# Kernel optimization log

Measured on AMD Instinct MI355X. Metric: run time of the kernel, lower is better.

Reference implementation:

```python
import jax, jax.numpy as jnp
import numpy as np

S, B, H, V, L = 128, 32, 512, 10000, 2

def setup_inputs() -> dict:
    key = jax.random.key(0)
    ks = jax.random.split(key, 8)
    u = float(np.sqrt(1.0 / H))
    return {
        "tokens": jax.random.randint(ks[0], (S, B), 0, V, dtype=jnp.int64),
        "h0": jnp.zeros((L, B, H), dtype=jnp.float32),
        "emb": jax.random.normal(ks[1], (V, H), dtype=jnp.float32) * 0.1,
        "Wx": jax.random.uniform(ks[2], (L, 3, H, H), minval=-u, maxval=u, dtype=jnp.float32),
        "bx": jax.random.uniform(ks[3], (L, 3, H), minval=-u, maxval=u, dtype=jnp.float32),
        "U": jax.random.uniform(ks[4], (L, 3, H, H), minval=-u, maxval=u, dtype=jnp.float32),
        "Wy": jax.random.uniform(ks[5], (V, H), minval=-u, maxval=u, dtype=jnp.float32),
        "by": jax.random.uniform(ks[6], (V,), minval=-u, maxval=u, dtype=jnp.float32),
    }

def _gru_cell(x, h, Wx, bx, U):
    # x,h: [B,H]; Wx,U: [3,H,H]; bx: [3,H]
    ax = jnp.einsum('bi,gio->bgo', x, Wx) + bx  # [B,3,H]
    r = jax.nn.sigmoid(ax[:, 0] + h @ U[0])
    z = jax.nn.sigmoid(ax[:, 1] + h @ U[1])
    h_hat = jnp.tanh(ax[:, 2] + (r * h) @ U[2])
    return (1.0 - z) * h + z * h_hat

def reference(tokens, h0, emb, Wx, bx, U, Wy, by):
    embs = emb[tokens]  # [S,B,H]

    def step(h_stack, x_t):
        new_h = []
        inp = x_t
        for l in range(L):
            h_l = _gru_cell(inp, h_stack[l], Wx[l], bx[l], U[l])
            new_h.append(h_l)
            inp = h_l
        return jnp.stack(new_h), inp  # carry, top-layer output

    h_final, tops = jax.lax.scan(step, h0, embs)  # tops: [S,B,H]
    logits = jnp.einsum('sbh,vh->sbv', tops, Wy) + by  # [S,B,V]
    return logits, h_final
```

## Files before the change

### kernel.cpp

```cpp
#include <hip/hip_runtime.h>
#include <cmath>

#define S_LEN 128
#define BATCH 32
#define HID   512
#define VOCAB 10000
#define MROWS (S_LEN * BATCH)
#define HH    (HID * HID)

#define NBLK  64
#define NTHR  512

typedef float f32x4 __attribute__((ext_vector_type(4)));

template<bool GATHER_A, bool B_KN, bool C_T>
__global__ __launch_bounds__(256) void gemm_kernel(
    const float* __restrict__ A, const int* __restrict__ tok,
    const float* __restrict__ Bmat, const float* __restrict__ bias,
    float* __restrict__ C, int M, int N, int K)
{
    __shared__ float As[32][68];
    __shared__ float Bs[32][68];
    __shared__ int   toks[64];

    const int tid = threadIdx.x;
    const int m0  = blockIdx.y * 64;
    const int n0  = blockIdx.x * 64;

    if (GATHER_A && tid < 64) toks[tid] = tok[m0 + tid];
    __syncthreads();

    const int tx = tid & 15;
    const int ty = tid >> 4;
    const int lr = tid >> 3;
    const int lc = (tid & 7) * 4;

    float acc[4][4] = {};

    for (int k0 = 0; k0 < K; k0 += 32) {
        #pragma unroll
        for (int rep = 0; rep < 2; rep++) {
            int r = lr + rep * 32;
            const float* arow;
            if (GATHER_A) arow = A + (size_t)toks[r] * K;
            else          arow = A + (size_t)(m0 + r) * K;
            float4 v = *(const float4*)(arow + k0 + lc);
            As[lc + 0][r] = v.x; As[lc + 1][r] = v.y;
            As[lc + 2][r] = v.z; As[lc + 3][r] = v.w;
        }
        if (B_KN) {
            int g    = n0 >> 9;
            int col0 = n0 & 511;
            const float* bbase = Bmat + (size_t)g * K * 512 + col0;
            int bc = (tid & 15) * 4;
            int bk = tid >> 4;
            #pragma unroll
            for (int rep = 0; rep < 2; rep++) {
                int kk = bk + rep * 16;
                float4 v = *(const float4*)(bbase + (size_t)(k0 + kk) * 512 + bc);
                *(float4*)&Bs[kk][bc] = v;
            }
        } else {
            #pragma unroll
            for (int rep = 0; rep < 2; rep++) {
                int r = lr + rep * 32;
                int n = n0 + r;
                float4 v = make_float4(0.f, 0.f, 0.f, 0.f);
                if (n < N) v = *(const float4*)(Bmat + (size_t)n * K + k0 + lc);
                Bs[lc + 0][r] = v.x; Bs[lc + 1][r] = v.y;
                Bs[lc + 2][r] = v.z; Bs[lc + 3][r] = v.w;
            }
        }
        __syncthreads();
        #pragma unroll
        for (int k = 0; k < 32; k++) {
            float4 a4 = *(const float4*)&As[k][ty * 4];
            float4 b4 = *(const float4*)&Bs[k][tx * 4];
            float av[4] = {a4.x, a4.y, a4.z, a4.w};
            float bv[4] = {b4.x, b4.y, b4.z, b4.w};
            #pragma unroll
            for (int i = 0; i < 4; i++)
                #pragma unroll
                for (int j = 0; j < 4; j++)
                    acc[i][j] = fmaf(av[i], bv[j], acc[i][j]);
        }
        __syncthreads();
    }
    if (C_T) {
        #pragma unroll
        for (int j = 0; j < 4; j++) {
            int n = n0 + tx * 4 + j;
            float bn = bias[n];
            float4 v = make_float4(acc[0][j] + bn, acc[1][j] + bn,
                                   acc[2][j] + bn, acc[3][j] + bn);
            *(float4*)&C[(size_t)n * M + m0 + ty * 4] = v;
        }
    } else {
        #pragma unroll
        for (int i = 0; i < 4; i++) {
            int m = m0 + ty * 4 + i;
            #pragma unroll
            for (int j = 0; j < 4; j++) {
                int n = n0 + tx * 4 + j;
                if (n < N) C[(size_t)m * N + n] = acc[i][j] + bias[n];
            }
        }
    }
}

__global__ __launch_bounds__(256) void gemm128_kernel(
    const float* __restrict__ A, const float* __restrict__ B,
    const float* __restrict__ bias, float* __restrict__ C,
    int M, int N, int K)
{
    __shared__ float As[16][132];
    __shared__ float Bs[16][132];

    const int tid = threadIdx.x;
    const int m0  = blockIdx.y * 128;
    const int n0  = blockIdx.x * 128;
    const int tx  = tid & 15;
    const int ty  = tid >> 4;
    const int lr  = tid >> 2;
    const int lc  = (tid & 3) * 4;

    float acc[8][8] = {};

    for (int k0 = 0; k0 < K; k0 += 16) {
        #pragma unroll
        for (int rep = 0; rep < 2; rep++) {
            int r = lr + rep * 64;
            float4 va = *(const float4*)(A + (size_t)(m0 + r) * K + k0 + lc);
            As[lc + 0][r] = va.x; As[lc + 1][r] = va.y;
            As[lc + 2][r] = va.z; As[lc + 3][r] = va.w;
            int n = n0 + r;
            float4 vb = make_float4(0.f, 0.f, 0.f, 0.f);
            if (n < N) vb = *(const float4*)(B + (size_t)n * K + k0 + lc);
            Bs[lc + 0][r] = vb.x; Bs[lc + 1][r] = vb.y;
            Bs[lc + 2][r] = vb.z; Bs[lc + 3][r] = vb.w;
        }
        __syncthreads();
        #pragma unroll
        for (int k = 0; k < 16; k++) {
            f32x4 a0 = *(const f32x4*)&As[k][ty * 8];
            f32x4 a1 = *(const f32x4*)&As[k][ty * 8 + 4];
            f32x4 b0 = *(const f32x4*)&Bs[k][tx * 8];
            f32x4 b1 = *(const f32x4*)&Bs[k][tx * 8 + 4];
            float av[8] = {a0.x,a0.y,a0.z,a0.w,a1.x,a1.y,a1.z,a1.w};
            float bv[8] = {b0.x,b0.y,b0.z,b0.w,b1.x,b1.y,b1.z,b1.w};
            #pragma unroll
            for (int i = 0; i < 8; i++)
                #pragma unroll
                for (int j = 0; j < 8; j++)
                    acc[i][j] = fmaf(av[i], bv[j], acc[i][j]);
        }
        __syncthreads();
    }
    const bool full = (n0 + 128 <= N);
    #pragma unroll
    for (int i = 0; i < 8; i++) {
        int m = m0 + ty * 8 + i;
        if (full) {
            int n = n0 + tx * 8;
            float4 v0 = make_float4(acc[i][0]+bias[n+0], acc[i][1]+bias[n+1],
                                    acc[i][2]+bias[n+2], acc[i][3]+bias[n+3]);
            float4 v1 = make_float4(acc[i][4]+bias[n+4], acc[i][5]+bias[n+5],
                                    acc[i][6]+bias[n+6], acc[i][7]+bias[n+7]);
            *(float4*)&C[(size_t)m * N + n]     = v0;
            *(float4*)&C[(size_t)m * N + n + 4] = v1;
        } else {
            #pragma unroll
            for (int j = 0; j < 8; j++) {
                int n = n0 + tx * 8 + j;
                if (n < N) C[(size_t)m * N + n] = acc[i][j] + bias[n];
            }
        }
    }
}

__device__ __forceinline__ f32x4 ldg_coh_x4(const float* p) {
    f32x4 r;
    asm volatile("global_load_dwordx4 %0, %1, off sc1"
                 : "=v"(r) : "v"(p) : "memory");
    return r;
}
__device__ __forceinline__ void stg_coh(float* p, float v) {
    asm volatile("global_store_dword %0, %1, off sc1"
                 :: "v"(p), "v"(v) : "memory");
}

__device__ __forceinline__ void bar_arrive(unsigned* flags, int bid, unsigned target)
{
    asm volatile("s_waitcnt vmcnt(0)" ::: "memory");
    __syncthreads();
    if (threadIdx.x == 0)
        __hip_atomic_store(&flags[bid], target, __ATOMIC_RELEASE, __HIP_MEMORY_SCOPE_AGENT);
}
__device__ __forceinline__ void bar_wait(unsigned* flags, unsigned target)
{
    if (threadIdx.x < NBLK) {
        while (__hip_atomic_load(&flags[threadIdx.x], __ATOMIC_RELAXED,
                                 __HIP_MEMORY_SCOPE_AGENT) < target)
            __builtin_amdgcn_s_sleep(1);
    }
    __syncthreads();
}

__global__ __launch_bounds__(NTHR) void scan_coop_kernel(
    const float* __restrict__ axT, const float* __restrict__ Ul,
    const float* __restrict__ h0g, float* __restrict__ hseq,
    float* __restrict__ hfin, float* __restrict__ vT,
    float* __restrict__ hxT, unsigned* __restrict__ flags)
{
    __shared__ float Wr[512 * 8];
    __shared__ float Wz[512 * 8];
    __shared__ float Wh[512 * 8];
    __shared__ float xbuf[512 * 32];
    __shared__ float part[32 * 256];
    __shared__ float partR[8 * 256];
    __shared__ float zbuf[8 * 33];
    __shared__ float hsave[8 * 33];
    __shared__ float hnb[8 * 33];

    const int tid = threadIdx.x;
    const int bid = blockIdx.x;
    const int ch0 = bid << 3;

    const int bt  = tid & 7;
    const int ct1 = (tid >> 3) & 1;
    const int ks  = tid >> 4;
    const int wsel = ((ct1 ^ ks) & 1) << 2;
    const int rc  = tid >> 5;
    const int rb  = tid & 31;

    for (int idx = tid; idx < 512 * 8; idx += NTHR) {
        int c = idx & 7, k = idx >> 3;
        int p = (k << 3) + ((((c >> 2) ^ (k >> 4)) & 1) << 2) + (c & 3);
        Wr[p] = Ul[                (size_t)k * HID + ch0 + c];
        Wz[p] = Ul[(size_t)1 * HH + (size_t)k * HID + ch0 + c];
        Wh[p] = Ul[(size_t)2 * HH + (size_t)k * HID + ch0 + c];
    }

    if (tid < 256)
        stg_coh(hxT + (ch0 + rc) * 32 + rb, h0g[rb * HID + ch0 + rc]);
    unsigned bc = 1;
    bar_arrive(flags, bid, bc);

    float axr = 0.f, axz = 0.f, axh = 0.f;
    if (tid < 256) {
        axr = axT[(size_t)(       ch0 + rc) * MROWS + rb];
        axz = axT[(size_t)( 512 + ch0 + rc) * MROWS + rb];
        axh = axT[(size_t)(1024 + ch0 + rc) * MROWS + rb];
    }
    bar_wait(flags, bc); bc++;

    for (int t = 0; t < S_LEN; t++) {
        {
            f32x4 ld[8];
            #pragma unroll
            for (int i = 0; i < 8; i++)
                ld[i] = ldg_coh_x4(hxT + (size_t)(tid + i * NTHR) * 4);
            asm volatile("s_waitcnt vmcnt(0)" ::: "memory");
            #pragma unroll
            for (int i = 0; i < 8; i++)
                *(f32x4*)&xbuf[(tid + i * NTHR) * 4] = ld[i];
        }
        __syncthreads();

        {
            f32x4 a0 = {0.f,0.f,0.f,0.f}, a1 = a0, a2 = a0, a3 = a0;
            const int kb = ks << 4;
            #pragma unroll
            for (int kk = 0; kk < 16; kk++) {
                int k = kb + kk;
                f32x4 wv = *(const f32x4*)&Wr[(k << 3) + wsel];
                f32x4 xv = *(const f32x4*)&xbuf[(k << 5) + (bt << 2)];
                a0 += wv.x * xv; a1 += wv.y * xv;
                a2 += wv.z * xv; a3 += wv.w * xv;
            }
            const int c0 = ct1 << 2;
            *(f32x4*)&part[(ks << 8) + ((c0    ) << 5) + (bt << 2)] = a0;
            *(f32x4*)&part[(ks << 8) + ((c0 + 1) << 5) + (bt << 2)] = a1;
            *(f32x4*)&part[(ks << 8) + ((c0 + 2) << 5) + (bt << 2)] = a2;
            *(f32x4*)&part[(ks << 8) + ((c0 + 3) << 5) + (bt << 2)] = a3;
        }
        __syncthreads();
        {
            const int out4 = tid & 63, qh = tid >> 6;
            f32x4 s = {0.f,0.f,0.f,0.f};
            #pragma unroll
            for (int j = 0; j < 4; j++)
                s += *(const f32x4*)&part[(((qh << 2) + j) << 8) + (out4 << 2)];
            *(f32x4*)&partR[(qh << 8) + (out4 << 2)] = s;
        }
        __syncthreads();
        if (tid < 256) {
            float s = 0.f;
            #pragma unroll
            for (int qh = 0; qh < 8; qh++) s += partR[(qh << 8) + (rc << 5) + rb];
            float sig = 1.f / (1.f + __expf(-(axr + s)));
            float hk  = xbuf[((ch0 + rc) << 5) + rb];
            stg_coh(vT + (ch0 + rc) * 32 + rb, sig * hk);
        }
        bar_arrive(flags, bid, bc);

        {
            f32x4 a0 = {0.f,0.f,0.f,0.f}, a1 = a0, a2 = a0, a3 = a0;
            const int kb = ks << 4;
            #pragma unroll
            for (int kk = 0; kk < 16; kk++) {
                int k = kb + kk;
                f32x4 wv = *(const f32x4*)&Wz[(k << 3) + wsel];
                f32x4 xv = *(const f32x4*)&xbuf[(k << 5) + (bt << 2)];
                a0 += wv.x * xv; a1 += wv.y * xv;
                a2 += wv.z * xv; a3 += wv.w * xv;
            }
            const int c0 = ct1 << 2;
            *(f32x4*)&part[(ks << 8) + ((c0    ) << 5) + (bt << 2)] = a0;
            *(f32x4*)&part[(ks << 8) + ((c0 + 1) << 5) + (bt << 2)] = a1;
            *(f32x4*)&part[(ks << 8) + ((c0 + 2) << 5) + (bt << 2)] = a2;
            *(f32x4*)&part[(ks << 8) + ((c0 + 3) << 5) + (bt << 2)] = a3;
        }
        __syncthreads();
        {
            const int out4 = tid & 63, qh = tid >> 6;
            f32x4 s = {0.f,0.f,0.f,0.f};
            #pragma unroll
            for (int j = 0; j < 4; j++)
                s += *(const f32x4*)&part[(((qh << 2) + j) << 8) + (out4 << 2)];
            *(f32x4*)&partR[(qh << 8) + (out4 << 2)] = s;
        }
        __syncthreads();
        if (tid < 256) {
            float s = 0.f;
            #pragma unroll
            for (int qh = 0; qh < 8; qh++) s += partR[(qh << 8) + (rc << 5) + rb];
            zbuf[rc * 33 + rb]  = 1.f / (1.f + __expf(-(axz + s)));
            hsave[rc * 33 + rb] = xbuf[((ch0 + rc) << 5) + rb];
        }
        bar_wait(flags, bc); bc++;

        {
            f32x4 ld[8];
            #pragma unroll
            for (int i = 0; i < 8; i++)
                ld[i] = ldg_coh_x4(vT + (size_t)(tid + i * NTHR) * 4);
            asm volatile("s_waitcnt vmcnt(0)" ::: "memory");
            #pragma unroll
            for (int i = 0; i < 8; i++)
                *(f32x4*)&xbuf[(tid + i * NTHR) * 4] = ld[i];
        }
        __syncthreads();

        {
            f32x4 a0 = {0.f,0.f,0.f,0.f}, a1 = a0, a2 = a0, a3 = a0;
            const int kb = ks << 4;
            #pragma unroll
            for (int kk = 0; kk < 16; kk++) {
                int k = kb + kk;
                f32x4 wv = *(const f32x4*)&Wh[(k << 3) + wsel];
                f32x4 xv = *(const f32x4*)&xbuf[(k << 5) + (bt << 2)];
                a0 += wv.x * xv; a1 += wv.y * xv;
                a2 += wv.z * xv; a3 += wv.w * xv;
            }
            const int c0 = ct1 << 2;
            *(f32x4*)&part[(ks << 8) + ((c0    ) << 5) + (bt << 2)] = a0;
            *(f32x4*)&part[(ks << 8) + ((c0 + 1) << 5) + (bt << 2)] = a1;
            *(f32x4*)&part[(ks << 8) + ((c0 + 2) << 5) + (bt << 2)] = a2;
            *(f32x4*)&part[(ks << 8) + ((c0 + 3) << 5) + (bt << 2)] = a3;
        }
        __syncthreads();
        {
            const int out4 = tid & 63, qh = tid >> 6;
            f32x4 s = {0.f,0.f,0.f,0.f};
            #pragma unroll
            for (int j = 0; j < 4; j++)
                s += *(const f32x4*)&part[(((qh << 2) + j) << 8) + (out4 << 2)];
            *(f32x4*)&partR[(qh << 8) + (out4 << 2)] = s;
        }
        __syncthreads();
        if (tid < 256) {
            float s = 0.f;
            #pragma unroll
            for (int qh = 0; qh < 8; qh++) s += partR[(qh << 8) + (rc << 5) + rb];
            float pre = axh + s;
            float e2  = __expf(2.f * pre);
            float hh  = 1.f - 2.f / (e2 + 1.f);
            float z   = zbuf[rc * 33 + rb];
            float h   = hsave[rc * 33 + rb];
            float hn  = (1.f - z) * h + z * hh;
            stg_coh(hxT + (ch0 + rc) * 32 + rb, hn);
            hnb[rc * 33 + rb] = hn;
            if (t == S_LEN - 1) hfin[rb * HID + ch0 + rc] = hn;
        }
        bar_arrive(flags, bid, bc);

        if (tid < 256) {
            const int c2 = tid & 7, b2 = tid >> 3;
            hseq[(size_t)((t << 5) + b2) * HID + ch0 + c2] = hnb[c2 * 33 + b2];
            if (t + 1 < S_LEN) {
                const size_t o = (size_t)((t + 1) << 5) + rb;
                axr = axT[(size_t)(       ch0 + rc) * MROWS + o];
                axz = axT[(size_t)( 512 + ch0 + rc) * MROWS + o];
                axh = axT[(size_t)(1024 + ch0 + rc) * MROWS + o];
            }
        }
        bar_wait(flags, bc); bc++;
    }
}

extern "C" void kernel_launch(void* const* d_in, const int* in_sizes, int n_in,
                              void* d_out, int out_size, void* d_ws, size_t ws_size,
                              hipStream_t stream)
{
    const int*   tokens = (const int*)  d_in[0];
    const float* h0     = (const float*)d_in[1];
    const float* emb    = (const float*)d_in[2];
    const float* Wx     = (const float*)d_in[3];
    const float* bx     = (const float*)d_in[4];
    const float* U      = (const float*)d_in[5];
    const float* Wy     = (const float*)d_in[6];
    const float* by     = (const float*)d_in[7];
    float*       out    = (float*)d_out;

    float* ws    = (float*)d_ws;
    float* axT   = ws;
    float* hseq  = axT + (size_t)1536 * MROWS;

    const size_t logits_sz = (size_t)MROWS * VOCAB;
    float* hfin0 = out + logits_sz;
    float* hfin1 = out + logits_sz + BATCH * HID;

    float*    vT    = out;
    float*    hxT   = out + 16384;
    unsigned* flags = (unsigned*)(out + 32768);
    hipMemsetAsync(flags, 0, 2 * NBLK * sizeof(unsigned), stream);

    gemm_kernel<true, true, true><<<dim3(1536 / 64, MROWS / 64), 256, 0, stream>>>(
        emb, tokens, Wx, bx, axT, MROWS, 1536, HID);

    scan_coop_kernel<<<NBLK, NTHR, 0, stream>>>(
        axT, U, h0, hseq, hfin0, vT, hxT, flags);

    gemm_kernel<false, true, true><<<dim3(1536 / 64, MROWS / 64), 256, 0, stream>>>(
        hseq, nullptr, Wx + 3 * HH, bx + 1536, axT, MROWS, 1536, HID);

    scan_coop_kernel<<<NBLK, NTHR, 0, stream>>>(
        axT, U + 3 * HH, h0 + BATCH * HID, hseq, hfin1, vT, hxT, flags + NBLK);

    gemm128_kernel<<<dim3((VOCAB + 127) / 128, MROWS / 128), 256, 0, stream>>>(
        hseq, Wy, by, out, MROWS, VOCAB, HID);
}
```

Before: 3.453 ms.

## Spread recurrent scan over 128 blocks and unify GEMMs on swizzled 128x128 tiles

The cooperative scan kernel now runs on 128 blocks that each own 4 hidden channels instead of 64 blocks owning 8. Each block does half the recurrent dot-product work per step, and the reductions are reorganized into 64 k-slices. The input-projection GEMMs move from 64x64 to 128x128 tiles via one templated kernel, with an XOR swizzle on the B shared-memory tile to reduce bank conflicts. The wider scan increases the number of blocks polling the flag barrier each step, and the larger GEMM tiles launch fewer blocks.

```diff
diff --git a/kernel.cpp b/kernel.cpp
--- a/kernel.cpp
+++ b/kernel.cpp
@@ -8,144 +8,84 @@
 #define MROWS (S_LEN * BATCH)
 #define HH    (HID * HID)
 
-#define NBLK  64
+#define NBLK  128
 #define NTHR  512
 
 typedef float f32x4 __attribute__((ext_vector_type(4)));
 
 template<bool GATHER_A, bool B_KN, bool C_T>
-__global__ __launch_bounds__(256) void gemm_kernel(
+__global__ __launch_bounds__(256) void gemm128_kernel(
     const float* __restrict__ A, const int* __restrict__ tok,
     const float* __restrict__ Bmat, const float* __restrict__ bias,
     float* __restrict__ C, int M, int N, int K)
 {
-    __shared__ float As[32][68];
-    __shared__ float Bs[32][68];
-    __shared__ int   toks[64];
+    __shared__ float As[16][132];
+    __shared__ float Bs[16][132];
+    __shared__ int   toks[128];
 
     const int tid = threadIdx.x;
-    const int m0  = blockIdx.y * 64;
-    const int n0  = blockIdx.x * 64;
-
-    if (GATHER_A && tid < 64) toks[tid] = tok[m0 + tid];
-    __syncthreads();
+    const int m0  = blockIdx.y * 128;
+    const int n0  = blockIdx.x * 128;
+
+    if (GATHER_A) {
+        if (tid < 128) toks[tid] = tok[m0 + tid];
+        __syncthreads();
+    }
 
     const int tx = tid & 15;
     const int ty = tid >> 4;
-    const int lr = tid >> 3;
-    const int lc = (tid & 7) * 4;
-
-    float acc[4][4] = {};
-
-    for (int k0 = 0; k0 < K; k0 += 32) {
+    const int lr = tid >> 2;
+    const int lc = (tid & 3) * 4;
+
+    const int qb   = tx << 1;
+    const int bbit = (qb >> 3) & 1;
+    const int bq0  = ((qb    ) ^ bbit) << 2;
+    const int bq1  = ((qb + 1) ^ bbit) << 2;
+
+    float acc[8][8] = {};
+
+    for (int k0 = 0; k0 < K; k0 += 16) {
         #pragma unroll
         for (int rep = 0; rep < 2; rep++) {
-            int r = lr + rep * 32;
-            const float* arow;
-            if (GATHER_A) arow = A + (size_t)toks[r] * K;
-            else          arow = A + (size_t)(m0 + r) * K;
-            float4 v = *(const float4*)(arow + k0 + lc);
-            As[lc + 0][r] = v.x; As[lc + 1][r] = v.y;
-            As[lc + 2][r] = v.z; As[lc + 3][r] = v.w;
+            int r = lr + rep * 64;
+            const float* arow = GATHER_A ? A + (size_t)toks[r] * K
+                                         : A + (size_t)(m0 + r) * K;
+            float4 va = *(const float4*)(arow + k0 + lc);
+            As[lc + 0][r] = va.x; As[lc + 1][r] = va.y;
+            As[lc + 2][r] = va.z; As[lc + 3][r] = va.w;
         }
         if (B_KN) {
-            int g    = n0 >> 9;
-            int col0 = n0 & 511;
-            const float* bbase = Bmat + (size_t)g * K * 512 + col0;
-            int bc = (tid & 15) * 4;
-            int bk = tid >> 4;
+            const int g = n0 >> 9, col0 = n0 & 511;
+            const float* bb = Bmat + (size_t)g * K * 512 + col0;
+            const int q  = tid & 31;
+            const int pq = (q ^ ((q >> 3) & 1)) << 2;
+            const int bkh = tid >> 5;
             #pragma unroll
             for (int rep = 0; rep < 2; rep++) {
-                int kk = bk + rep * 16;
-                float4 v = *(const float4*)(bbase + (size_t)(k0 + kk) * 512 + bc);
-                *(float4*)&Bs[kk][bc] = v;
+                int kk = bkh + rep * 8;
+                float4 vb = *(const float4*)(bb + (size_t)(k0 + kk) * 512 + q * 4);
+                *(float4*)&Bs[kk][pq] = vb;
             }
         } else {
             #pragma unroll
             for (int rep = 0; rep < 2; rep++) {
-                int r = lr + rep * 32;
+                int r = lr + rep * 64;
                 int n = n0 + r;
-                float4 v = make_float4(0.f, 0.f, 0.f, 0.f);
-                if (n < N) v = *(const float4*)(Bmat + (size_t)n * K + k0 + lc);
-                Bs[lc + 0][r] = v.x; Bs[lc + 1][r] = v.y;
-                Bs[lc + 2][r] = v.z; Bs[lc + 3][r] = v.w;
+                float4 vb = make_float4(0.f, 0.f, 0.f, 0.f);
+                if (n < N) vb = *(const float4*)(Bmat + (size_t)n * K + k0 + lc);
+                int q  = r >> 2;
+                int pc = ((q ^ ((q >> 3) & 1)) << 2) + (r & 3);
+                Bs[lc + 0][pc] = vb.x; Bs[lc + 1][pc] = vb.y;
+                Bs[lc + 2][pc] = vb.z; Bs[lc + 3][pc] = vb.w;
             }
-        }
-        __syncthreads();
-        #pragma unroll
-        for (int k = 0; k < 32; k++) {
-            float4 a4 = *(const float4*)&As[k][ty * 4];
-            float4 b4 = *(const float4*)&Bs[k][tx * 4];
-            float av[4] = {a4.x, a4.y, a4.z, a4.w};
-            float bv[4] = {b4.x, b4.y, b4.z, b4.w};
-            #pragma unroll
-            for (int i = 0; i < 4; i++)
-                #pragma unroll
-                for (int j = 0; j < 4; j++)
-                    acc[i][j] = fmaf(av[i], bv[j], acc[i][j]);
-        }
-        __syncthreads();
-    }
-    if (C_T) {
-        #pragma unroll
-        for (int j = 0; j < 4; j++) {
-            int n = n0 + tx * 4 + j;
-            float bn = bias[n];
-            float4 v = make_float4(acc[0][j] + bn, acc[1][j] + bn,
-                                   acc[2][j] + bn, acc[3][j] + bn);
-            *(float4*)&C[(size_t)n * M + m0 + ty * 4] = v;
-        }
-    } else {
-        #pragma unroll
-        for (int i = 0; i < 4; i++) {
-            int m = m0 + ty * 4 + i;
-            #pragma unroll
-            for (int j = 0; j < 4; j++) {
-                int n = n0 + tx * 4 + j;
-                if (n < N) C[(size_t)m * N + n] = acc[i][j] + bias[n];
-            }
-        }
-    }
-}
-
-__global__ __launch_bounds__(256) void gemm128_kernel(
-    const float* __restrict__ A, const float* __restrict__ B,
-    const float* __restrict__ bias, float* __restrict__ C,
-    int M, int N, int K)
-{
-    __shared__ float As[16][132];
-    __shared__ float Bs[16][132];
-
-    const int tid = threadIdx.x;
-    const int m0  = blockIdx.y * 128;
-    const int n0  = blockIdx.x * 128;
-    const int tx  = tid & 15;
-    const int ty  = tid >> 4;
-    const int lr  = tid >> 2;
-    const int lc  = (tid & 3) * 4;
-
-    float acc[8][8] = {};
-
-    for (int k0 = 0; k0 < K; k0 += 16) {
-        #pragma unroll
-        for (int rep = 0; rep < 2; rep++) {
-            int r = lr + rep * 64;
-            float4 va = *(const float4*)(A + (size_t)(m0 + r) * K + k0 + lc);
-            As[lc + 0][r] = va.x; As[lc + 1][r] = va.y;
-            As[lc + 2][r] = va.z; As[lc + 3][r] = va.w;
-            int n = n0 + r;
-            float4 vb = make_float4(0.f, 0.f, 0.f, 0.f);
-            if (n < N) vb = *(const float4*)(B + (size_t)n * K + k0 + lc);
-            Bs[lc + 0][r] = vb.x; Bs[lc + 1][r] = vb.y;
-            Bs[lc + 2][r] = vb.z; Bs[lc + 3][r] = vb.w;
         }
         __syncthreads();
         #pragma unroll
         for (int k = 0; k < 16; k++) {
             f32x4 a0 = *(const f32x4*)&As[k][ty * 8];
             f32x4 a1 = *(const f32x4*)&As[k][ty * 8 + 4];
-            f32x4 b0 = *(const f32x4*)&Bs[k][tx * 8];
-            f32x4 b1 = *(const f32x4*)&Bs[k][tx * 8 + 4];
+            f32x4 b0 = *(const f32x4*)&Bs[k][bq0];
+            f32x4 b1 = *(const f32x4*)&Bs[k][bq1];
             float av[8] = {a0.x,a0.y,a0.z,a0.w,a1.x,a1.y,a1.z,a1.w};
             float bv[8] = {b0.x,b0.y,b0.z,b0.w,b1.x,b1.y,b1.z,b1.w};
             #pragma unroll
@@ -156,23 +96,38 @@
         }
         __syncthreads();
     }
-    const bool full = (n0 + 128 <= N);
-    #pragma unroll
-    for (int i = 0; i < 8; i++) {
-        int m = m0 + ty * 8 + i;
-        if (full) {
-            int n = n0 + tx * 8;
-            float4 v0 = make_float4(acc[i][0]+bias[n+0], acc[i][1]+bias[n+1],
-                                    acc[i][2]+bias[n+2], acc[i][3]+bias[n+3]);
-            float4 v1 = make_float4(acc[i][4]+bias[n+4], acc[i][5]+bias[n+5],
-                                    acc[i][6]+bias[n+6], acc[i][7]+bias[n+7]);
-            *(float4*)&C[(size_t)m * N + n]     = v0;
-            *(float4*)&C[(size_t)m * N + n + 4] = v1;
-        } else {
-            #pragma unroll
-            for (int j = 0; j < 8; j++) {
-                int n = n0 + tx * 8 + j;
-                if (n < N) C[(size_t)m * N + n] = acc[i][j] + bias[n];
+    if (C_T) {
+        #pragma unroll
+        for (int j = 0; j < 8; j++) {
+            int n = n0 + tx * 8 + j;
+            float bn_ = bias[n];
+            float4 v0 = make_float4(acc[0][j]+bn_, acc[1][j]+bn_,
+                                    acc[2][j]+bn_, acc[3][j]+bn_);
+            float4 v1 = make_float4(acc[4][j]+bn_, acc[5][j]+bn_,
+                                    acc[6][j]+bn_, acc[7][j]+bn_);
+            float* cp = C + (size_t)n * M + m0 + ty * 8;
+            *(float4*)cp       = v0;
+            *(float4*)(cp + 4) = v1;
+        }
+    } else {
+        const bool full = (n0 + 128 <= N);
+        #pragma unroll
+        for (int i = 0; i < 8; i++) {
+            int m = m0 + ty * 8 + i;
+            if (full) {
+                int n = n0 + tx * 8;
+                float4 v0 = make_float4(acc[i][0]+bias[n+0], acc[i][1]+bias[n+1],
+                                        acc[i][2]+bias[n+2], acc[i][3]+bias[n+3]);
+                float4 v1 = make_float4(acc[i][4]+bias[n+4], acc[i][5]+bias[n+5],
+                                        acc[i][6]+bias[n+6], acc[i][7]+bias[n+7]);
+                *(float4*)&C[(size_t)m * N + n]     = v0;
+                *(float4*)&C[(size_t)m * N + n + 4] = v1;
+            } else {
+                #pragma unroll
+                for (int j = 0; j < 8; j++) {
+                    int n = n0 + tx * 8 + j;
+                    if (n < N) C[(size_t)m * N + n] = acc[i][j] + bias[n];
+                }
             }
         }
     }
@@ -212,177 +167,123 @@
     float* __restrict__ hfin, float* __restrict__ vT,
     float* __restrict__ hxT, unsigned* __restrict__ flags)
 {
-    __shared__ float Wr[512 * 8];
-    __shared__ float Wz[512 * 8];
-    __shared__ float Wh[512 * 8];
-    __shared__ float xbuf[512 * 32];
-    __shared__ float part[32 * 256];
-    __shared__ float partR[8 * 256];
-    __shared__ float zbuf[8 * 33];
-    __shared__ float hsave[8 * 33];
-    __shared__ float hnb[8 * 33];
+    __shared__ float Wr[HID * 4];
+    __shared__ float Wz[HID * 4];
+    __shared__ float Wh[HID * 4];
+    __shared__ float xbuf[HID * 32];
+    __shared__ float part[64 * 128];
+    __shared__ float partR[16 * 128];
+    __shared__ float zbuf[4 * 33];
+    __shared__ float hsave[4 * 33];
+    __shared__ float hnb[4 * 33];
 
     const int tid = threadIdx.x;
     const int bid = blockIdx.x;
-    const int ch0 = bid << 3;
-
-    const int bt  = tid & 7;
-    const int ct1 = (tid >> 3) & 1;
-    const int ks  = tid >> 4;
-    const int wsel = ((ct1 ^ ks) & 1) << 2;
-    const int rc  = tid >> 5;
-    const int rb  = tid & 31;
-
-    for (int idx = tid; idx < 512 * 8; idx += NTHR) {
-        int c = idx & 7, k = idx >> 3;
-        int p = (k << 3) + ((((c >> 2) ^ (k >> 4)) & 1) << 2) + (c & 3);
-        Wr[p] = Ul[                (size_t)k * HID + ch0 + c];
-        Wz[p] = Ul[(size_t)1 * HH + (size_t)k * HID + ch0 + c];
-        Wh[p] = Ul[(size_t)2 * HH + (size_t)k * HID + ch0 + c];
-    }
-
-    if (tid < 256)
+    const int ch0 = bid << 2;
+
+    const int bt   = tid & 7;
+    const int ks   = tid >> 3;
+    const int out4 = tid & 31;
+    const int qh   = tid >> 5;
+    const int rc   = tid >> 5;
+    const int rb   = tid & 31;
+
+    for (int idx = tid; idx < HID * 4; idx += NTHR) {
+        int c = idx & 3, k = idx >> 2;
+        Wr[idx] = Ul[                 (size_t)k * HID + ch0 + c];
+        Wz[idx] = Ul[(size_t)1 * HH + (size_t)k * HID + ch0 + c];
+        Wh[idx] = Ul[(size_t)2 * HH + (size_t)k * HID + ch0 + c];
+    }
+
+    if (tid < 128)
         stg_coh(hxT + (ch0 + rc) * 32 + rb, h0g[rb * HID + ch0 + rc]);
     unsigned bc = 1;
     bar_arrive(flags, bid, bc);
 
     float axr = 0.f, axz = 0.f, axh = 0.f;
-    if (tid < 256) {
+    if (tid < 128) {
         axr = axT[(size_t)(       ch0 + rc) * MROWS + rb];
         axz = axT[(size_t)( 512 + ch0 + rc) * MROWS + rb];
         axh = axT[(size_t)(1024 + ch0 + rc) * MROWS + rb];
     }
     bar_wait(flags, bc); bc++;
 
+#define DOT(W) {                                                          \
+    f32x4 a0 = {0.f,0.f,0.f,0.f}, a1 = a0, a2 = a0, a3 = a0;              \
+    const float* wb = (W) + (ks << 5);                                    \
+    const float* xb = xbuf + (ks << 8) + (bt << 2);                       \
+    _Pragma("unroll")                                                     \
+    for (int kk = 0; kk < 8; kk++) {                                      \
+        f32x4 wv = *(const f32x4*)(wb + (kk << 2));                       \
+        f32x4 xv = *(const f32x4*)(xb + (kk << 5));                       \
+        a0 += wv.x * xv; a1 += wv.y * xv;                                 \
+        a2 += wv.z * xv; a3 += wv.w * xv;                                 \
+    }                                                                     \
+    float* pp = part + (ks << 7) + (bt << 2);                             \
+    *(f32x4*)(pp     ) = a0;                                              \
+    *(f32x4*)(pp + 32) = a1;                                              \
+    *(f32x4*)(pp + 64) = a2;                                              \
+    *(f32x4*)(pp + 96) = a3; }
+
+#define RED1 {                                                            \
+    f32x4 s = {0.f,0.f,0.f,0.f};                                          \
+    _Pragma("unroll")                                                     \
+    for (int jj = 0; jj < 4; jj++)                                        \
+        s += *(const f32x4*)&part[(((qh << 2) + jj) << 7) + (out4 << 2)]; \
+    *(f32x4*)&partR[(qh << 7) + (out4 << 2)] = s; }
+
+#define RED2(dst) {                                                       \
+    float s_ = 0.f;                                                       \
+    _Pragma("unroll")                                                     \
+    for (int q_ = 0; q_ < 16; q_++) s_ += partR[(q_ << 7) + tid];         \
+    dst = s_; }
+
+#define STAGE(src) {                                                      \
+    f32x4 ld[8];                                                          \
+    _Pragma("unroll")                                                     \
+    for (int i = 0; i < 8; i++)                                           \
+        ld[i] = ldg_coh_x4((src) + (size_t)(tid + i * NTHR) * 4);         \
+    asm volatile("s_waitcnt vmcnt(0)" ::: "memory");                      \
+    _Pragma("unroll")                                                     \
+    for (int i = 0; i < 8; i++)                                           \
+        *(f32x4*)&xbuf[(tid + i * NTHR) * 4] = ld[i]; }
+
     for (int t = 0; t < S_LEN; t++) {
-        {
-            f32x4 ld[8];
-            #pragma unroll
-            for (int i = 0; i < 8; i++)
-                ld[i] = ldg_coh_x4(hxT + (size_t)(tid + i * NTHR) * 4);
-            asm volatile("s_waitcnt vmcnt(0)" ::: "memory");
-            #pragma unroll
-            for (int i = 0; i < 8; i++)
-                *(f32x4*)&xbuf[(tid + i * NTHR) * 4] = ld[i];
-        }
-        __syncthreads();
-
-        {
-            f32x4 a0 = {0.f,0.f,0.f,0.f}, a1 = a0, a2 = a0, a3 = a0;
-            const int kb = ks << 4;
-            #pragma unroll
-            for (int kk = 0; kk < 16; kk++) {
-                int k = kb + kk;
-                f32x4 wv = *(const f32x4*)&Wr[(k << 3) + wsel];
-                f32x4 xv = *(const f32x4*)&xbuf[(k << 5) + (bt << 2)];
-                a0 += wv.x * xv; a1 += wv.y * xv;
-                a2 += wv.z * xv; a3 += wv.w * xv;
-            }
-            const int c0 = ct1 << 2;
-            *(f32x4*)&part[(ks << 8) + ((c0    ) << 5) + (bt << 2)] = a0;
-            *(f32x4*)&part[(ks << 8) + ((c0 + 1) << 5) + (bt << 2)] = a1;
-            *(f32x4*)&part[(ks << 8) + ((c0 + 2) << 5) + (bt << 2)] = a2;
-            *(f32x4*)&part[(ks << 8) + ((c0 + 3) << 5) + (bt << 2)] = a3;
-        }
-        __syncthreads();
-        {
-            const int out4 = tid & 63, qh = tid >> 6;
-            f32x4 s = {0.f,0.f,0.f,0.f};
-            #pragma unroll
-            for (int j = 0; j < 4; j++)
-                s += *(const f32x4*)&part[(((qh << 2) + j) << 8) + (out4 << 2)];
-            *(f32x4*)&partR[(qh << 8) + (out4 << 2)] = s;
-        }
-        __syncthreads();
-        if (tid < 256) {
-            float s = 0.f;
-            #pragma unroll
-            for (int qh = 0; qh < 8; qh++) s += partR[(qh << 8) + (rc << 5) + rb];
+        STAGE(hxT);
+        __syncthreads();
+
+        DOT(Wr);
+        __syncthreads();
+        RED1;
+        __syncthreads();
+        if (tid < 128) {
+            float s; RED2(s);
             float sig = 1.f / (1.f + __expf(-(axr + s)));
             float hk  = xbuf[((ch0 + rc) << 5) + rb];
             stg_coh(vT + (ch0 + rc) * 32 + rb, sig * hk);
         }
         bar_arrive(flags, bid, bc);
 
-        {
-            f32x4 a0 = {0.f,0.f,0.f,0.f}, a1 = a0, a2 = a0, a3 = a0;
-            const int kb = ks << 4;
-            #pragma unroll
-            for (int kk = 0; kk < 16; kk++) {
-                int k = kb + kk;
-                f32x4 wv = *(const f32x4*)&Wz[(k << 3) + wsel];
-                f32x4 xv = *(const f32x4*)&xbuf[(k << 5) + (bt << 2)];
-                a0 += wv.x * xv; a1 += wv.y * xv;
-                a2 += wv.z * xv; a3 += wv.w * xv;
-            }
-            const int c0 = ct1 << 2;
-            *(f32x4*)&part[(ks << 8) + ((c0    ) << 5) + (bt << 2)] = a0;
-            *(f32x4*)&part[(ks << 8) + ((c0 + 1) << 5) + (bt << 2)] = a1;
-            *(f32x4*)&part[(ks << 8) + ((c0 + 2) << 5) + (bt << 2)] = a2;
-            *(f32x4*)&part[(ks << 8) + ((c0 + 3) << 5) + (bt << 2)] = a3;
-        }
-        __syncthreads();
-        {
-            const int out4 = tid & 63, qh = tid >> 6;
-            f32x4 s = {0.f,0.f,0.f,0.f};
-            #pragma unroll
-            for (int j = 0; j < 4; j++)
-                s += *(const f32x4*)&part[(((qh << 2) + j) << 8) + (out4 << 2)];
-            *(f32x4*)&partR[(qh << 8) + (out4 << 2)] = s;
-        }
-        __syncthreads();
-        if (tid < 256) {
-            float s = 0.f;
-            #pragma unroll
-            for (int qh = 0; qh < 8; qh++) s += partR[(qh << 8) + (rc << 5) + rb];
+        DOT(Wz);
+        __syncthreads();
+        RED1;
+        __syncthreads();
+        if (tid < 128) {
+            float s; RED2(s);
             zbuf[rc * 33 + rb]  = 1.f / (1.f + __expf(-(axz + s)));
             hsave[rc * 33 + rb] = xbuf[((ch0 + rc) << 5) + rb];
         }
         bar_wait(flags, bc); bc++;
 
-        {
-            f32x4 ld[8];
-            #pragma unroll
-            for (int i = 0; i < 8; i++)
-                ld[i] = ldg_coh_x4(vT + (size_t)(tid + i * NTHR) * 4);
-            asm volatile("s_waitcnt vmcnt(0)" ::: "memory");
-            #pragma unroll
-            for (int i = 0; i < 8; i++)
-                *(f32x4*)&xbuf[(tid + i * NTHR) * 4] = ld[i];
-        }
-        __syncthreads();
-
-        {
-            f32x4 a0 = {0.f,0.f,0.f,0.f}, a1 = a0, a2 = a0, a3 = a0;
-            const int kb = ks << 4;
-            #pragma unroll
-            for (int kk = 0; kk < 16; kk++) {
-                int k = kb + kk;
-                f32x4 wv = *(const f32x4*)&Wh[(k << 3) + wsel];
-                f32x4 xv = *(const f32x4*)&xbuf[(k << 5) + (bt << 2)];
-                a0 += wv.x * xv; a1 += wv.y * xv;
-                a2 += wv.z * xv; a3 += wv.w * xv;
-            }
-            const int c0 = ct1 << 2;
-            *(f32x4*)&part[(ks << 8) + ((c0    ) << 5) + (bt << 2)] = a0;
-            *(f32x4*)&part[(ks << 8) + ((c0 + 1) << 5) + (bt << 2)] = a1;
-            *(f32x4*)&part[(ks << 8) + ((c0 + 2) << 5) + (bt << 2)] = a2;
-            *(f32x4*)&part[(ks << 8) + ((c0 + 3) << 5) + (bt << 2)] = a3;
-        }
-        __syncthreads();
-        {
-            const int out4 = tid & 63, qh = tid >> 6;
-            f32x4 s = {0.f,0.f,0.f,0.f};
-            #pragma unroll
-            for (int j = 0; j < 4; j++)
-                s += *(const f32x4*)&part[(((qh << 2) + j) << 8) + (out4 << 2)];
-            *(f32x4*)&partR[(qh << 8) + (out4 << 2)] = s;
-        }
-        __syncthreads();
-        if (tid < 256) {
-            float s = 0.f;
-            #pragma unroll
-            for (int qh = 0; qh < 8; qh++) s += partR[(qh << 8) + (rc << 5) + rb];
+        STAGE(vT);
+        __syncthreads();
+
+        DOT(Wh);
+        __syncthreads();
+        RED1;
+        __syncthreads();
+        if (tid < 128) {
+            float s; RED2(s);
             float pre = axh + s;
             float e2  = __expf(2.f * pre);
             float hh  = 1.f - 2.f / (e2 + 1.f);
@@ -395,8 +296,8 @@
         }
         bar_arrive(flags, bid, bc);
 
-        if (tid < 256) {
-            const int c2 = tid & 7, b2 = tid >> 3;
+        if (tid < 128) {
+            const int c2 = tid & 3, b2 = tid >> 2;
             hseq[(size_t)((t << 5) + b2) * HID + ch0 + c2] = hnb[c2 * 33 + b2];
             if (t + 1 < S_LEN) {
                 const size_t o = (size_t)((t + 1) << 5) + rb;
@@ -407,6 +308,10 @@
         }
         bar_wait(flags, bc); bc++;
     }
+#undef DOT
+#undef RED1
+#undef RED2
+#undef STAGE
 }
 
 extern "C" void kernel_launch(void* const* d_in, const int* in_sizes, int n_in,
@@ -436,18 +341,18 @@
     unsigned* flags = (unsigned*)(out + 32768);
     hipMemsetAsync(flags, 0, 2 * NBLK * sizeof(unsigned), stream);
 
-    gemm_kernel<true, true, true><<<dim3(1536 / 64, MROWS / 64), 256, 0, stream>>>(
+    gemm128_kernel<true, true, true><<<dim3(1536 / 128, MROWS / 128), 256, 0, stream>>>(
         emb, tokens, Wx, bx, axT, MROWS, 1536, HID);
 
     scan_coop_kernel<<<NBLK, NTHR, 0, stream>>>(
         axT, U, h0, hseq, hfin0, vT, hxT, flags);
 
-    gemm_kernel<false, true, true><<<dim3(1536 / 64, MROWS / 64), 256, 0, stream>>>(
+    gemm128_kernel<false, true, true><<<dim3(1536 / 128, MROWS / 128), 256, 0, stream>>>(
         hseq, nullptr, Wx + 3 * HH, bx + 1536, axT, MROWS, 1536, HID);
 
     scan_coop_kernel<<<NBLK, NTHR, 0, stream>>>(
         axT, U + 3 * HH, h0 + BATCH * HID, hseq, hfin1, vT, hxT, flags + NBLK);
 
-    gemm128_kernel<<<dim3((VOCAB + 127) / 128, MROWS / 128), 256, 0, stream>>>(
-        hseq, Wy, by, out, MROWS, VOCAB, HID);
-}
+    gemm128_kernel<false, false, false><<<dim3((VOCAB + 127) / 128, MROWS / 128), 256, 0, stream>>>(
+        hseq, nullptr, Wy, by, out, MROWS, VOCAB, HID);
+}
```

New measurement: 4.519 ms. 1.31x slower.
